# Optimization experiments

Hardware: AMD Instinct MI355X
Metric: run time of the kernel (lower is better)

The kernel has to match this reference:

```python
import jax, jax.numpy as jnp
import numpy as np

N, E, DIN, DOUT, EDIM = 100000, 1000000, 64, 64, 64


def _xavier(k, shape, gain=1.0):
    fan_out, fan_in = shape
    a = gain * np.sqrt(6.0 / (fan_in + fan_out))
    return jax.random.uniform(k, shape, jnp.float32, -a, a)


def setup_inputs() -> dict:
    key = jax.random.key(0)
    ks = jax.random.split(key, 16)
    relu_gain = float(np.sqrt(2.0))  # nn.init.calculate_gain('relu')
    return {
        "nfeats": jax.random.normal(ks[0], (N, DIN), jnp.float32),
        "efeats": jax.random.normal(ks[1], (E, EDIM), jnp.float32),
        "src": jax.random.randint(ks[2], (E,), 0, N),
        "dst": jax.random.randint(ks[3], (E,), 0, N),
        "e_perm": jax.random.permutation(ks[4], E),
        # layer 0 params (torch Linear layout: [out, in])
        "Wmsg0": _xavier(ks[5], (DOUT, DIN + EDIM)),
        "bmsg0": jnp.zeros((DOUT,), jnp.float32),
        "Wapply0": _xavier(ks[6], (DOUT, DIN + DOUT), relu_gain),
        "bapply0": jnp.zeros((DOUT,), jnp.float32),
        # layer 1 params
        "Wmsg1": _xavier(ks[7], (DOUT, DOUT + EDIM)),
        "bmsg1": jnp.zeros((DOUT,), jnp.float32),
        "Wapply1": _xavier(ks[8], (DOUT, DOUT + DOUT), relu_gain),
        "bapply1": jnp.zeros((DOUT,), jnp.float32),
    }


def _sage_layer(h, ef, src, dst, Wmsg, bmsg, Wap, bap, n_nodes):
    # message: W_msg(cat(src_h, e_h)) per edge  -> [E, dout]
    m = jnp.concatenate([h[src], ef], axis=1) @ Wmsg.T + bmsg
    # mean-reduce messages onto destination nodes
    s = jax.ops.segment_sum(m, dst, num_segments=n_nodes)
    cnt = jax.ops.segment_sum(jnp.ones((dst.shape[0],), m.dtype), dst, num_segments=n_nodes)
    h_neigh = s / jnp.maximum(cnt, 1.0)[:, None]  # zero-in-degree nodes -> 0
    return jax.nn.relu(jnp.concatenate([h, h_neigh], axis=1) @ Wap.T + bap)


def _bce_with_logits(x, target):
    # mean(log(1+exp(x)) - x*target), numerically stable via logaddexp
    return jnp.mean(jnp.logaddexp(0.0, x) - x * target)


def reference(nfeats, efeats, src, dst, e_perm,
              Wmsg0, bmsg0, Wapply0, bapply0,
              Wmsg1, bmsg1, Wapply1, bapply1):
    n_nodes = nfeats.shape[0]

    def encode(ef):
        h = _sage_layer(nfeats, ef, src, dst, Wmsg0, bmsg0, Wapply0, bapply0, n_nodes)
        h = _sage_layer(h, ef, src, dst, Wmsg1, bmsg1, Wapply1, bapply1, n_nodes)
        return h

    positive = encode(efeats)
    negative = encode(efeats[e_perm])  # corrupted view: permuted edge features
    P_LABEL, N_LABEL = 1.0, 0.0  # DGI p / n targets
    return _bce_with_logits(positive, P_LABEL) + _bce_with_logits(negative, N_LABEL)
```

## Files before the change

kernel.cpp:

```cpp
#include <hip/hip_runtime.h>
#include <math.h>

#define NN 100000
#define NE 1000000
#define D  64
#define NB_SCAN 391


__global__ __launch_bounds__(256) void k_hist(
    const int* __restrict__ dst, int* __restrict__ counts, int* __restrict__ rank)
{
    int e = blockIdx.x * 256 + threadIdx.x;
    if (e >= NE) return;
    rank[e] = atomicAdd(&counts[dst[e]], 1);
}

__global__ __launch_bounds__(256) void k_scan1(
    const int* __restrict__ counts, int* __restrict__ row_start, int* __restrict__ bsum)
{
    __shared__ int s[256];
    int t = threadIdx.x;
    int i = blockIdx.x * 256 + t;
    int v = (i < NN) ? counts[i] : 0;
    s[t] = v; __syncthreads();
#pragma unroll
    for (int off = 1; off < 256; off <<= 1) {
        int add = (t >= off) ? s[t - off] : 0;
        __syncthreads();
        s[t] += add;
        __syncthreads();
    }
    if (i < NN) row_start[i] = s[t] - v;
    if (t == 255) bsum[blockIdx.x] = s[255];
}

__global__ __launch_bounds__(512) void k_scan2(
    const int* __restrict__ bsum, int* __restrict__ boff, int* __restrict__ row_start)
{
    __shared__ int s[512];
    int t = threadIdx.x;
    int v = (t < NB_SCAN) ? bsum[t] : 0;
    s[t] = v; __syncthreads();
#pragma unroll
    for (int off = 1; off < 512; off <<= 1) {
        int add = (t >= off) ? s[t - off] : 0;
        __syncthreads();
        s[t] += add;
        __syncthreads();
    }
    if (t < NB_SCAN) boff[t] = s[t] - v;
    if (t == 0) row_start[NN] = NE;
}

__global__ __launch_bounds__(256) void k_scan3(
    int* __restrict__ row_start, const int* __restrict__ boff)
{
    int i = blockIdx.x * 256 + threadIdx.x;
    if (i < NN) row_start[i] += boff[i >> 8];
}

__global__ __launch_bounds__(256) void k_scatter(
    const int* __restrict__ dst, const int* __restrict__ src,
    const int* __restrict__ perm, const int* __restrict__ rank,
    const int* __restrict__ row_start, int4* __restrict__ sorted)
{
    int e = blockIdx.x * 256 + threadIdx.x;
    if (e >= NE) return;
    int pos = row_start[dst[e]] + rank[e];
    sorted[pos] = make_int4(src[e], e, perm[e], 0);
}


__global__ __launch_bounds__(256) void pull_pass1(
    const int4* __restrict__ sorted, const int* __restrict__ row_start,
    const float* __restrict__ nfeats, const float* __restrict__ efeats,
    float* __restrict__ hsum0, float* __restrict__ efsP, float* __restrict__ efsN)
{
    int gt = blockIdx.x * 256 + threadIdx.x;
    int w = gt >> 6, lane = gt & 63;
    if (w >= NN) return;
    int es = lane >> 4, c4 = (lane & 15) << 2;
    int beg = row_start[w], end = row_start[w + 1];

    float an0 = 0.f, an1 = 0.f, an2 = 0.f, an3 = 0.f;
    float ap0 = 0.f, ap1 = 0.f, ap2 = 0.f, ap3 = 0.f;
    float ag0 = 0.f, ag1 = 0.f, ag2 = 0.f, ag3 = 0.f;
    int i = beg + es;
    int4 q = (i < end) ? sorted[i] : make_int4(0, 0, 0, 0);
#pragma unroll 1
    for (; i < end; i += 4) {
        int inext = i + 4;
        int4 qn = (inext < end) ? sorted[inext] : make_int4(0, 0, 0, 0);
        float4 n  = *(const float4*)(nfeats + (size_t)q.x * D + c4);
        float4 ep = *(const float4*)(efeats + (size_t)q.y * D + c4);
        float4 en = *(const float4*)(efeats + (size_t)q.z * D + c4);
        an0 += n.x;  an1 += n.y;  an2 += n.z;  an3 += n.w;
        ap0 += ep.x; ap1 += ep.y; ap2 += ep.z; ap3 += ep.w;
        ag0 += en.x; ag1 += en.y; ag2 += en.z; ag3 += en.w;
        q = qn;
    }
#pragma unroll
    for (int off = 16; off <= 32; off <<= 1) {
        an0 += __shfl_xor(an0, off, 64); an1 += __shfl_xor(an1, off, 64);
        an2 += __shfl_xor(an2, off, 64); an3 += __shfl_xor(an3, off, 64);
        ap0 += __shfl_xor(ap0, off, 64); ap1 += __shfl_xor(ap1, off, 64);
        ap2 += __shfl_xor(ap2, off, 64); ap3 += __shfl_xor(ap3, off, 64);
        ag0 += __shfl_xor(ag0, off, 64); ag1 += __shfl_xor(ag1, off, 64);
        ag2 += __shfl_xor(ag2, off, 64); ag3 += __shfl_xor(ag3, off, 64);
    }
    if (lane < 16) {
        *(float4*)(hsum0 + (size_t)w * D + c4) = make_float4(an0, an1, an2, an3);
        *(float4*)(efsP  + (size_t)w * D + c4) = make_float4(ap0, ap1, ap2, ap3);
        *(float4*)(efsN  + (size_t)w * D + c4) = make_float4(ag0, ag1, ag2, ag3);
    }
}

__global__ __launch_bounds__(256) void pull_h2(
    const int4* __restrict__ sorted, const int* __restrict__ row_start,
    const float* __restrict__ hP, const float* __restrict__ hN,
    float* __restrict__ hsumP, float* __restrict__ hsumN)
{
    int gt = blockIdx.x * 256 + threadIdx.x;
    int w = gt >> 6, lane = gt & 63;
    if (w >= NN) return;
    int es = lane >> 4, c4 = (lane & 15) << 2;
    int beg = row_start[w], end = row_start[w + 1];

    float p0 = 0.f, p1 = 0.f, p2 = 0.f, p3 = 0.f;
    float n0 = 0.f, n1 = 0.f, n2 = 0.f, n3 = 0.f;
    int i = beg + es;
    int s = (i < end) ? sorted[i].x : 0;
#pragma unroll 1
    for (; i < end; i += 4) {
        int inext = i + 4;
        int sn = (inext < end) ? sorted[inext].x : 0;
        float4 vP = *(const float4*)(hP + (size_t)s * D + c4);
        float4 vN = *(const float4*)(hN + (size_t)s * D + c4);
        p0 += vP.x; p1 += vP.y; p2 += vP.z; p3 += vP.w;
        n0 += vN.x; n1 += vN.y; n2 += vN.z; n3 += vN.w;
        s = sn;
    }
#pragma unroll
    for (int off = 16; off <= 32; off <<= 1) {
        p0 += __shfl_xor(p0, off, 64); p1 += __shfl_xor(p1, off, 64);
        p2 += __shfl_xor(p2, off, 64); p3 += __shfl_xor(p3, off, 64);
        n0 += __shfl_xor(n0, off, 64); n1 += __shfl_xor(n1, off, 64);
        n2 += __shfl_xor(n2, off, 64); n3 += __shfl_xor(n3, off, 64);
    }
    if (lane < 16) {
        *(float4*)(hsumP + (size_t)w * D + c4) = make_float4(p0, p1, p2, p3);
        *(float4*)(hsumN + (size_t)w * D + c4) = make_float4(n0, n1, n2, n3);
    }
}


__device__ __forceinline__ void gemm_half(
    float acc[4][4], const float (*As)[68], const float (*Bs)[68],
    int ty, int tx4, int hb)
{
#pragma unroll 1
    for (int k0 = 0; k0 < 64; k0 += 4) {
        float a[4][4];
#pragma unroll
        for (int i = 0; i < 4; ++i)
            *(float4*)&a[i][0] = *(const float4*)&As[ty + 16 * i][k0];
#pragma unroll
        for (int kk = 0; kk < 4; ++kk) {
            float4 b = *(const float4*)&Bs[hb + k0 + kk][tx4];
#pragma unroll
            for (int i = 0; i < 4; ++i) {
                acc[i][0] += a[i][kk] * b.x;
                acc[i][1] += a[i][kk] * b.y;
                acc[i][2] += a[i][kk] * b.z;
                acc[i][3] += a[i][kk] * b.w;
            }
        }
    }
}

#define STAGE_A(SRC) { \
    _Pragma("unroll") \
    for (int g = 0; g < 4; ++g) { \
        int idx = g * 256 + tid; \
        int node = idx >> 4, c = (idx & 15) << 2; \
        int gn = block0 + node; \
        float4 v = make_float4(0.f, 0.f, 0.f, 0.f); \
        if (gn < NN) v = *(const float4*)((SRC) + (size_t)gn * D + c); \
        *(float4*)&As[node][c] = v; } }

#define STAGE_B(W) { \
    _Pragma("unroll 1") \
    for (int i = 0; i < 32; ++i) { \
        int idx = i * 256 + tid; \
        Bs[idx & 127][idx >> 7] = (W)[idx]; } }

#define STORE_MSG(M) { \
    _Pragma("unroll") \
    for (int i = 0; i < 4; ++i) \
        *(float4*)&As[ty + 16 * i][tx4] = make_float4((M)[i][0], (M)[i][1], (M)[i][2], (M)[i][3]); }

__global__ __launch_bounds__(256, 4) void fused2_l0(
    const float* __restrict__ Hsum, const float* __restrict__ EsumP,
    const float* __restrict__ EsumN, const float* __restrict__ Hprev,
    const int* __restrict__ counts,
    const float* __restrict__ Wmsg, const float* __restrict__ bmsg,
    const float* __restrict__ Wap, const float* __restrict__ bap,
    float* __restrict__ HoutP, float* __restrict__ HoutN)
{
    __shared__ __align__(16) float As[64][68];
    __shared__ __align__(16) float Bs[128][68];
    int tid = threadIdx.x;
    int block0 = blockIdx.x * 64;
    int tx = tid & 15, ty = tid >> 4;
    int tx4 = tx << 2;

    float cnt[4], inv[4];
#pragma unroll
    for (int i = 0; i < 4; ++i) {
        int gn = block0 + ty + 16 * i;
        cnt[i] = (gn < NN) ? (float)counts[gn] : 0.f;
        inv[i] = 1.0f / fmaxf(cnt[i], 1.0f);
    }
    float bm[4], ba[4];
#pragma unroll
    for (int j = 0; j < 4; ++j) { bm[j] = bmsg[tx4 + j]; ba[j] = bap[tx4 + j]; }

    STAGE_B(Wmsg);
    STAGE_A(Hsum);
    __syncthreads();
    float accb[4][4] = {};
    gemm_half(accb, As, Bs, ty, tx4, 0);
    __syncthreads();
    STAGE_A(EsumP);
    __syncthreads();
    float msgP[4][4];
#pragma unroll
    for (int i = 0; i < 4; ++i)
#pragma unroll
        for (int j = 0; j < 4; ++j) msgP[i][j] = accb[i][j];
    gemm_half(msgP, As, Bs, ty, tx4, 64);
#pragma unroll
    for (int i = 0; i < 4; ++i)
#pragma unroll
        for (int j = 0; j < 4; ++j) msgP[i][j] = (msgP[i][j] + cnt[i] * bm[j]) * inv[i];
    __syncthreads();
    STAGE_A(EsumN);
    __syncthreads();
    gemm_half(accb, As, Bs, ty, tx4, 64);
    float msgN[4][4];
#pragma unroll
    for (int i = 0; i < 4; ++i)
#pragma unroll
        for (int j = 0; j < 4; ++j) msgN[i][j] = (accb[i][j] + cnt[i] * bm[j]) * inv[i];

    __syncthreads();
    STAGE_B(Wap);
    STAGE_A(Hprev);
    __syncthreads();
    float acc2b[4][4] = {};
    gemm_half(acc2b, As, Bs, ty, tx4, 0);

    __syncthreads();
    STORE_MSG(msgP);
    __syncthreads();
    float acc2[4][4];
#pragma unroll
    for (int i = 0; i < 4; ++i)
#pragma unroll
        for (int j = 0; j < 4; ++j) acc2[i][j] = acc2b[i][j];
    gemm_half(acc2, As, Bs, ty, tx4, 64);
#pragma unroll
    for (int i = 0; i < 4; ++i) {
        int gn = block0 + ty + 16 * i;
        if (gn >= NN) continue;
#pragma unroll
        for (int j = 0; j < 4; ++j)
            HoutP[(size_t)gn * D + tx4 + j] = fmaxf(acc2[i][j] + ba[j], 0.f);
    }

    __syncthreads();
    STORE_MSG(msgN);
    __syncthreads();
#pragma unroll
    for (int i = 0; i < 4; ++i)
#pragma unroll
        for (int j = 0; j < 4; ++j) acc2[i][j] = acc2b[i][j];
    gemm_half(acc2, As, Bs, ty, tx4, 64);
#pragma unroll
    for (int i = 0; i < 4; ++i) {
        int gn = block0 + ty + 16 * i;
        if (gn >= NN) continue;
#pragma unroll
        for (int j = 0; j < 4; ++j)
            HoutN[(size_t)gn * D + tx4 + j] = fmaxf(acc2[i][j] + ba[j], 0.f);
    }
}

__global__ __launch_bounds__(256, 4) void fused2_l1loss(
    const float* __restrict__ HsumP, const float* __restrict__ HsumN,
    const float* __restrict__ EsumP, const float* __restrict__ EsumN,
    const float* __restrict__ HprevP, const float* __restrict__ HprevN,
    const int* __restrict__ counts,
    const float* __restrict__ Wmsg, const float* __restrict__ bmsg,
    const float* __restrict__ Wap, const float* __restrict__ bap,
    float* __restrict__ loss_out)
{
    __shared__ __align__(16) float As[64][68];
    __shared__ __align__(16) float Bs[128][68];
    int tid = threadIdx.x;
    int block0 = blockIdx.x * 64;
    int tx = tid & 15, ty = tid >> 4;
    int tx4 = tx << 2;

    float cnt[4], inv[4];
#pragma unroll
    for (int i = 0; i < 4; ++i) {
        int gn = block0 + ty + 16 * i;
        cnt[i] = (gn < NN) ? (float)counts[gn] : 0.f;
        inv[i] = 1.0f / fmaxf(cnt[i], 1.0f);
    }
    float bm[4], ba[4];
#pragma unroll
    for (int j = 0; j < 4; ++j) { bm[j] = bmsg[tx4 + j]; ba[j] = bap[tx4 + j]; }

    float lsum = 0.f;
#pragma unroll 1
    for (int side = 0; side < 2; ++side) {
        const float* Hsum  = side ? HsumN  : HsumP;
        const float* Esum  = side ? EsumN  : EsumP;
        const float* Hprev = side ? HprevN : HprevP;

        if (side == 0) { STAGE_B(Wmsg); }
        else {
            __syncthreads();
            STAGE_B(Wmsg);
        }
        STAGE_A(Hsum);
        __syncthreads();
        float acc[4][4] = {};
        gemm_half(acc, As, Bs, ty, tx4, 0);
        __syncthreads();
        STAGE_A(Esum);
        __syncthreads();
        gemm_half(acc, As, Bs, ty, tx4, 64);
        float msg[4][4];
#pragma unroll
        for (int i = 0; i < 4; ++i)
#pragma unroll
            for (int j = 0; j < 4; ++j) msg[i][j] = (acc[i][j] + cnt[i] * bm[j]) * inv[i];

        __syncthreads();
        STAGE_B(Wap);
        STAGE_A(Hprev);
        __syncthreads();
        float acc2[4][4] = {};
        gemm_half(acc2, As, Bs, ty, tx4, 0);
        __syncthreads();
        STORE_MSG(msg);
        __syncthreads();
        gemm_half(acc2, As, Bs, ty, tx4, 64);

#pragma unroll
        for (int i = 0; i < 4; ++i) {
            int gn = block0 + ty + 16 * i;
            if (gn >= NN) continue;
#pragma unroll
            for (int j = 0; j < 4; ++j) {
                float x = fmaxf(acc2[i][j] + ba[j], 0.f);
                float l = log1pf(expf(-x));
                if (side) l += x;
                lsum += l;
            }
        }
    }
#pragma unroll
    for (int off = 32; off; off >>= 1) lsum += __shfl_down(lsum, off, 64);
    if ((tid & 63) == 0)
        unsafeAtomicAdd(loss_out, lsum * (1.0f / 6400000.0f));
}

extern "C" void kernel_launch(void* const* d_in, const int* in_sizes, int n_in,
                              void* d_out, int out_size, void* d_ws, size_t ws_size,
                              hipStream_t stream) {
    (void)in_sizes; (void)n_in; (void)out_size; (void)ws_size;
    const float* nfeats = (const float*)d_in[0];
    const float* efeats = (const float*)d_in[1];
    const int*   src    = (const int*)d_in[2];
    const int*   dst    = (const int*)d_in[3];
    const int*   perm   = (const int*)d_in[4];
    const float* Wmsg0  = (const float*)d_in[5];
    const float* bmsg0  = (const float*)d_in[6];
    const float* Wap0   = (const float*)d_in[7];
    const float* bap0   = (const float*)d_in[8];
    const float* Wmsg1  = (const float*)d_in[9];
    const float* bmsg1  = (const float*)d_in[10];
    const float* Wap1   = (const float*)d_in[11];
    const float* bap1   = (const float*)d_in[12];
    float* out = (float*)d_out;

    const size_t NV = (size_t)NN * D;
    char* p = (char*)d_ws;
    int4* sorted   = (int4*)p;               p += (size_t)NE * 16;
    int*  rank     = (int*)p;                p += (size_t)NE * 4;
    int*  counts   = (int*)p;                p += ((NN + 15) & ~15) * 4;
    int*  rowst    = (int*)p;                p += ((NN + 16) & ~15) * 4;
    int*  bsum     = (int*)p;                p += 512 * 4;
    int*  boff     = (int*)p;                p += 512 * 4;
    float* efsP    = (float*)p;              p += NV * 4;
    float* efsN    = (float*)p;              p += NV * 4;
    float* hsum0   = (float*)p;              p += NV * 4;
    float* h1P     = (float*)p;              p += NV * 4;
    float* h1N     = (float*)p;              p += NV * 4;
    float* hsum1P  = (float*)p;              p += NV * 4;
    float* hsum1N  = (float*)p;              p += NV * 4;

    const int EGb = (NE + 255) / 256;
    const int PGb = ((size_t)NN * 64 + 255) / 256;
    const int NG  = (NN + 63) / 64;

    hipMemsetAsync(counts, 0, (size_t)NN * 4, stream);
    hipMemsetAsync(d_out, 0, 4, stream);

    k_hist<<<EGb, 256, 0, stream>>>(dst, counts, rank);
    k_scan1<<<NB_SCAN, 256, 0, stream>>>(counts, rowst, bsum);
    k_scan2<<<1, 512, 0, stream>>>(bsum, boff, rowst);
    k_scan3<<<NB_SCAN, 256, 0, stream>>>(rowst, boff);
    k_scatter<<<EGb, 256, 0, stream>>>(dst, src, perm, rank, rowst, sorted);

    pull_pass1<<<PGb, 256, 0, stream>>>(sorted, rowst, nfeats, efeats, hsum0, efsP, efsN);

    fused2_l0<<<NG, 256, 0, stream>>>(hsum0, efsP, efsN, nfeats, counts,
                                      Wmsg0, bmsg0, Wap0, bap0, h1P, h1N);

    pull_h2<<<PGb, 256, 0, stream>>>(sorted, rowst, h1P, h1N, hsum1P, hsum1N);

    fused2_l1loss<<<NG, 256, 0, stream>>>(hsum1P, hsum1N, efsP, efsN, h1P, h1N,
                                          counts, Wmsg1, bmsg1, Wap1, bap1, out);
}
```

Before: 912.9 us.

## Pre-transpose weights once and read GEMM operands directly from global memory

Adds a small kernel that transposes the four weight matrices into a k-major layout once per call. The fused node GEMM kernels drop the shared-memory B tile and most A staging, and each thread reads its A rows and B columns straight from global/L2. Only the message tile still goes through LDS. This removes the per-block 32-iteration strided weight staging, many barriers and about 35KB of LDS per block, which may raise occupancy. The cost is redundant global loads across threads, which now depend on L1/L2 hits instead of LDS reuse.

```diff
diff --git a/kernel.cpp b/kernel.cpp
--- a/kernel.cpp
+++ b/kernel.cpp
@@ -68,6 +68,20 @@
     if (e >= NE) return;
     int pos = row_start[dst[e]] + rank[e];
     sorted[pos] = make_int4(src[e], e, perm[e], 0);
+}
+
+__global__ __launch_bounds__(256) void k_wt4(
+    const float* __restrict__ W0, const float* __restrict__ W1,
+    const float* __restrict__ W2, const float* __restrict__ W3,
+    float* __restrict__ T0, float* __restrict__ T1,
+    float* __restrict__ T2, float* __restrict__ T3)
+{
+    int t = blockIdx.x * 256 + threadIdx.x;
+    int m = t >> 13, idx = t & 8191;
+    const float* W = (m == 0) ? W0 : (m == 1) ? W1 : (m == 2) ? W2 : W3;
+    float*       T = (m == 0) ? T0 : (m == 1) ? T1 : (m == 2) ? T2 : T3;
+    int j = idx >> 7, k = idx & 127;
+    T[k * 64 + j] = W[idx];
 }
 
 
@@ -154,70 +168,77 @@
 }
 
 
-__device__ __forceinline__ void gemm_half(
-    float acc[4][4], const float (*As)[68], const float (*Bs)[68],
-    int ty, int tx4, int hb)
-{
-#pragma unroll 1
+__device__ __forceinline__ void gemm_gg(
+    float acc[4][4], const float* const* Ap, const float* __restrict__ Bt)
+{
+#pragma unroll 2
     for (int k0 = 0; k0 < 64; k0 += 4) {
         float a[4][4];
+        float4 bv[4];
+#pragma unroll
+        for (int i = 0; i < 4; ++i)
+            *(float4*)&a[i][0] = *(const float4*)(Ap[i] + k0);
+#pragma unroll
+        for (int kk = 0; kk < 4; ++kk)
+            bv[kk] = *(const float4*)(Bt + (k0 + kk) * 64);
+#pragma unroll
+        for (int kk = 0; kk < 4; ++kk)
+#pragma unroll
+            for (int i = 0; i < 4; ++i) {
+                acc[i][0] += a[i][kk] * bv[kk].x;
+                acc[i][1] += a[i][kk] * bv[kk].y;
+                acc[i][2] += a[i][kk] * bv[kk].z;
+                acc[i][3] += a[i][kk] * bv[kk].w;
+            }
+    }
+}
+
+__device__ __forceinline__ void gemm_lg(
+    float acc[4][4], const float (*As)[68], int ty, const float* __restrict__ Bt)
+{
+#pragma unroll 2
+    for (int k0 = 0; k0 < 64; k0 += 4) {
+        float a[4][4];
+        float4 bv[4];
 #pragma unroll
         for (int i = 0; i < 4; ++i)
             *(float4*)&a[i][0] = *(const float4*)&As[ty + 16 * i][k0];
 #pragma unroll
-        for (int kk = 0; kk < 4; ++kk) {
-            float4 b = *(const float4*)&Bs[hb + k0 + kk][tx4];
+        for (int kk = 0; kk < 4; ++kk)
+            bv[kk] = *(const float4*)(Bt + (k0 + kk) * 64);
+#pragma unroll
+        for (int kk = 0; kk < 4; ++kk)
 #pragma unroll
             for (int i = 0; i < 4; ++i) {
-                acc[i][0] += a[i][kk] * b.x;
-                acc[i][1] += a[i][kk] * b.y;
-                acc[i][2] += a[i][kk] * b.z;
-                acc[i][3] += a[i][kk] * b.w;
+                acc[i][0] += a[i][kk] * bv[kk].x;
+                acc[i][1] += a[i][kk] * bv[kk].y;
+                acc[i][2] += a[i][kk] * bv[kk].z;
+                acc[i][3] += a[i][kk] * bv[kk].w;
             }
-        }
-    }
-}
-
-#define STAGE_A(SRC) { \
-    _Pragma("unroll") \
-    for (int g = 0; g < 4; ++g) { \
-        int idx = g * 256 + tid; \
-        int node = idx >> 4, c = (idx & 15) << 2; \
-        int gn = block0 + node; \
-        float4 v = make_float4(0.f, 0.f, 0.f, 0.f); \
-        if (gn < NN) v = *(const float4*)((SRC) + (size_t)gn * D + c); \
-        *(float4*)&As[node][c] = v; } }
-
-#define STAGE_B(W) { \
-    _Pragma("unroll 1") \
-    for (int i = 0; i < 32; ++i) { \
-        int idx = i * 256 + tid; \
-        Bs[idx & 127][idx >> 7] = (W)[idx]; } }
-
-#define STORE_MSG(M) { \
-    _Pragma("unroll") \
-    for (int i = 0; i < 4; ++i) \
-        *(float4*)&As[ty + 16 * i][tx4] = make_float4((M)[i][0], (M)[i][1], (M)[i][2], (M)[i][3]); }
-
-__global__ __launch_bounds__(256, 4) void fused2_l0(
+    }
+}
+
+__global__ __launch_bounds__(256, 4) void fused3_l0(
     const float* __restrict__ Hsum, const float* __restrict__ EsumP,
     const float* __restrict__ EsumN, const float* __restrict__ Hprev,
     const int* __restrict__ counts,
-    const float* __restrict__ Wmsg, const float* __restrict__ bmsg,
-    const float* __restrict__ Wap, const float* __restrict__ bap,
+    const float* __restrict__ WtM, const float* __restrict__ bmsg,
+    const float* __restrict__ WtA, const float* __restrict__ bap,
     float* __restrict__ HoutP, float* __restrict__ HoutN)
 {
     __shared__ __align__(16) float As[64][68];
-    __shared__ __align__(16) float Bs[128][68];
     int tid = threadIdx.x;
     int block0 = blockIdx.x * 64;
     int tx = tid & 15, ty = tid >> 4;
     int tx4 = tx << 2;
 
+    size_t off[4];
     float cnt[4], inv[4];
 #pragma unroll
     for (int i = 0; i < 4; ++i) {
         int gn = block0 + ty + 16 * i;
+        int rc = (gn < NN) ? gn : (NN - 1);
+        off[i] = (size_t)rc * D;
         cnt[i] = (gn < NN) ? (float)counts[gn] : 0.f;
         inv[i] = 1.0f / fmaxf(cnt[i], 1.0f);
     }
@@ -225,50 +246,43 @@
 #pragma unroll
     for (int j = 0; j < 4; ++j) { bm[j] = bmsg[tx4 + j]; ba[j] = bap[tx4 + j]; }
 
-    STAGE_B(Wmsg);
-    STAGE_A(Hsum);
-    __syncthreads();
+    const float* BtM = WtM + tx4;
+    const float* BtA = WtA + tx4;
+    const float* Ap[4];
+
     float accb[4][4] = {};
-    gemm_half(accb, As, Bs, ty, tx4, 0);
-    __syncthreads();
-    STAGE_A(EsumP);
-    __syncthreads();
+#pragma unroll
+    for (int i = 0; i < 4; ++i) Ap[i] = Hsum + off[i];
+    gemm_gg(accb, Ap, BtM);
+
     float msgP[4][4];
 #pragma unroll
     for (int i = 0; i < 4; ++i)
 #pragma unroll
         for (int j = 0; j < 4; ++j) msgP[i][j] = accb[i][j];
-    gemm_half(msgP, As, Bs, ty, tx4, 64);
+#pragma unroll
+    for (int i = 0; i < 4; ++i) Ap[i] = EsumP + off[i];
+    gemm_gg(msgP, Ap, BtM + 64 * 64);
 #pragma unroll
     for (int i = 0; i < 4; ++i)
 #pragma unroll
         for (int j = 0; j < 4; ++j) msgP[i][j] = (msgP[i][j] + cnt[i] * bm[j]) * inv[i];
-    __syncthreads();
-    STAGE_A(EsumN);
-    __syncthreads();
-    gemm_half(accb, As, Bs, ty, tx4, 64);
-    float msgN[4][4];
-#pragma unroll
-    for (int i = 0; i < 4; ++i)
-#pragma unroll
-        for (int j = 0; j < 4; ++j) msgN[i][j] = (accb[i][j] + cnt[i] * bm[j]) * inv[i];
-
-    __syncthreads();
-    STAGE_B(Wap);
-    STAGE_A(Hprev);
-    __syncthreads();
+#pragma unroll
+    for (int i = 0; i < 4; ++i)
+        *(float4*)&As[ty + 16 * i][tx4] = make_float4(msgP[i][0], msgP[i][1], msgP[i][2], msgP[i][3]);
+
     float acc2b[4][4] = {};
-    gemm_half(acc2b, As, Bs, ty, tx4, 0);
-
-    __syncthreads();
-    STORE_MSG(msgP);
+#pragma unroll
+    for (int i = 0; i < 4; ++i) Ap[i] = Hprev + off[i];
+    gemm_gg(acc2b, Ap, BtA);
+
     __syncthreads();
     float acc2[4][4];
 #pragma unroll
     for (int i = 0; i < 4; ++i)
 #pragma unroll
         for (int j = 0; j < 4; ++j) acc2[i][j] = acc2b[i][j];
-    gemm_half(acc2, As, Bs, ty, tx4, 64);
+    gemm_lg(acc2, As, ty, BtA + 64 * 64);
 #pragma unroll
     for (int i = 0; i < 4; ++i) {
         int gn = block0 + ty + 16 * i;
@@ -278,14 +292,24 @@
             HoutP[(size_t)gn * D + tx4 + j] = fmaxf(acc2[i][j] + ba[j], 0.f);
     }
 
+#pragma unroll
+    for (int i = 0; i < 4; ++i) Ap[i] = EsumN + off[i];
+    gemm_gg(accb, Ap, BtM + 64 * 64);
+#pragma unroll
+    for (int i = 0; i < 4; ++i)
+#pragma unroll
+        for (int j = 0; j < 4; ++j) accb[i][j] = (accb[i][j] + cnt[i] * bm[j]) * inv[i];
+
     __syncthreads();
-    STORE_MSG(msgN);
+#pragma unroll
+    for (int i = 0; i < 4; ++i)
+        *(float4*)&As[ty + 16 * i][tx4] = make_float4(accb[i][0], accb[i][1], accb[i][2], accb[i][3]);
     __syncthreads();
 #pragma unroll
     for (int i = 0; i < 4; ++i)
 #pragma unroll
         for (int j = 0; j < 4; ++j) acc2[i][j] = acc2b[i][j];
-    gemm_half(acc2, As, Bs, ty, tx4, 64);
+    gemm_lg(acc2, As, ty, BtA + 64 * 64);
 #pragma unroll
     for (int i = 0; i < 4; ++i) {
         int gn = block0 + ty + 16 * i;
@@ -296,32 +320,38 @@
     }
 }
 
-__global__ __launch_bounds__(256, 4) void fused2_l1loss(
+__global__ __launch_bounds__(256, 4) void fused3_l1loss(
     const float* __restrict__ HsumP, const float* __restrict__ HsumN,
     const float* __restrict__ EsumP, const float* __restrict__ EsumN,
     const float* __restrict__ HprevP, const float* __restrict__ HprevN,
     const int* __restrict__ counts,
-    const float* __restrict__ Wmsg, const float* __restrict__ bmsg,
-    const float* __restrict__ Wap, const float* __restrict__ bap,
+    const float* __restrict__ WtM, const float* __restrict__ bmsg,
+    const float* __restrict__ WtA, const float* __restrict__ bap,
     float* __restrict__ loss_out)
 {
     __shared__ __align__(16) float As[64][68];
-    __shared__ __align__(16) float Bs[128][68];
     int tid = threadIdx.x;
     int block0 = blockIdx.x * 64;
     int tx = tid & 15, ty = tid >> 4;
     int tx4 = tx << 2;
 
+    size_t off[4];
     float cnt[4], inv[4];
 #pragma unroll
     for (int i = 0; i < 4; ++i) {
         int gn = block0 + ty + 16 * i;
+        int rc = (gn < NN) ? gn : (NN - 1);
+        off[i] = (size_t)rc * D;
         cnt[i] = (gn < NN) ? (float)counts[gn] : 0.f;
         inv[i] = 1.0f / fmaxf(cnt[i], 1.0f);
     }
     float bm[4], ba[4];
 #pragma unroll
     for (int j = 0; j < 4; ++j) { bm[j] = bmsg[tx4 + j]; ba[j] = bap[tx4 + j]; }
+
+    const float* BtM = WtM + tx4;
+    const float* BtA = WtA + tx4;
+    const float* Ap[4];
 
     float lsum = 0.f;
 #pragma unroll 1
@@ -330,35 +360,30 @@
         const float* Esum  = side ? EsumN  : EsumP;
         const float* Hprev = side ? HprevN : HprevP;
 
-        if (side == 0) { STAGE_B(Wmsg); }
-        else {
-            __syncthreads();
-            STAGE_B(Wmsg);
-        }
-        STAGE_A(Hsum);
-        __syncthreads();
         float acc[4][4] = {};
-        gemm_half(acc, As, Bs, ty, tx4, 0);
-        __syncthreads();
-        STAGE_A(Esum);
-        __syncthreads();
-        gemm_half(acc, As, Bs, ty, tx4, 64);
+#pragma unroll
+        for (int i = 0; i < 4; ++i) Ap[i] = Hsum + off[i];
+        gemm_gg(acc, Ap, BtM);
+#pragma unroll
+        for (int i = 0; i < 4; ++i) Ap[i] = Esum + off[i];
+        gemm_gg(acc, Ap, BtM + 64 * 64);
         float msg[4][4];
 #pragma unroll
         for (int i = 0; i < 4; ++i)
 #pragma unroll
             for (int j = 0; j < 4; ++j) msg[i][j] = (acc[i][j] + cnt[i] * bm[j]) * inv[i];
 
-        __syncthreads();
-        STAGE_B(Wap);
-        STAGE_A(Hprev);
-        __syncthreads();
         float acc2[4][4] = {};
-        gemm_half(acc2, As, Bs, ty, tx4, 0);
-        __syncthreads();
-        STORE_MSG(msg);
-        __syncthreads();
-        gemm_half(acc2, As, Bs, ty, tx4, 64);
+#pragma unroll
+        for (int i = 0; i < 4; ++i) Ap[i] = Hprev + off[i];
+        gemm_gg(acc2, Ap, BtA);
+
+        __syncthreads();
+#pragma unroll
+        for (int i = 0; i < 4; ++i)
+            *(float4*)&As[ty + 16 * i][tx4] = make_float4(msg[i][0], msg[i][1], msg[i][2], msg[i][3]);
+        __syncthreads();
+        gemm_lg(acc2, As, ty, BtA + 64 * 64);
 
 #pragma unroll
         for (int i = 0; i < 4; ++i) {
@@ -374,7 +399,7 @@
         }
     }
 #pragma unroll
-    for (int off = 32; off; off >>= 1) lsum += __shfl_down(lsum, off, 64);
+    for (int off2 = 32; off2; off2 >>= 1) lsum += __shfl_down(lsum, off2, 64);
     if ((tid & 63) == 0)
         unsafeAtomicAdd(loss_out, lsum * (1.0f / 6400000.0f));
 }
@@ -413,6 +438,10 @@
     float* h1N     = (float*)p;              p += NV * 4;
     float* hsum1P  = (float*)p;              p += NV * 4;
     float* hsum1N  = (float*)p;              p += NV * 4;
+    float* wtM0    = (float*)p;              p += 8192 * 4;
+    float* wtA0    = (float*)p;              p += 8192 * 4;
+    float* wtM1    = (float*)p;              p += 8192 * 4;
+    float* wtA1    = (float*)p;              p += 8192 * 4;
 
     const int EGb = (NE + 255) / 256;
     const int PGb = ((size_t)NN * 64 + 255) / 256;
@@ -420,6 +449,8 @@
 
     hipMemsetAsync(counts, 0, (size_t)NN * 4, stream);
     hipMemsetAsync(d_out, 0, 4, stream);
+
+    k_wt4<<<128, 256, 0, stream>>>(Wmsg0, Wap0, Wmsg1, Wap1, wtM0, wtA0, wtM1, wtA1);
 
     k_hist<<<EGb, 256, 0, stream>>>(dst, counts, rank);
     k_scan1<<<NB_SCAN, 256, 0, stream>>>(counts, rowst, bsum);
@@ -429,11 +460,11 @@
 
     pull_pass1<<<PGb, 256, 0, stream>>>(sorted, rowst, nfeats, efeats, hsum0, efsP, efsN);
 
-    fused2_l0<<<NG, 256, 0, stream>>>(hsum0, efsP, efsN, nfeats, counts,
-                                      Wmsg0, bmsg0, Wap0, bap0, h1P, h1N);
+    fused3_l0<<<NG, 256, 0, stream>>>(hsum0, efsP, efsN, nfeats, counts,
+                                      wtM0, bmsg0, wtA0, bap0, h1P, h1N);
 
     pull_h2<<<PGb, 256, 0, stream>>>(sorted, rowst, h1P, h1N, hsum1P, hsum1N);
 
-    fused2_l1loss<<<NG, 256, 0, stream>>>(hsum1P, hsum1N, efsP, efsN, h1P, h1N,
-                                          counts, Wmsg1, bmsg1, Wap1, bap1, out);
-}
+    fused3_l1loss<<<NG, 256, 0, stream>>>(hsum1P, hsum1N, efsP, efsN, h1P, h1N,
+                                          counts, wtM1, bmsg1, wtA1, bap1, out);
+}
```

Result: slower. 1.015 ms (+11.1%).

## Pre-transpose weights once and stage half-sized B tiles to cut LDS

Applied to the files above, without the earlier changes.

Adds a small kernel that transposes all four weight matrices into a [k][j] layout in workspace once per call. The fused GEMM kernels then load each 64-row half of the weights with coalesced float4 copies into a B tile half the previous size, instead of doing strided scalar transposing stores of the full 128x64 matrix. This lowers LDS per block, which may raise occupancy, and makes weight staging cheaper. The cost is extra syncs and restaging between halves, and one more kernel launch. The inner GEMM loop also preloads four B vectors ahead of the FMAs.

```diff
diff --git a/kernel.cpp b/kernel.cpp
--- a/kernel.cpp
+++ b/kernel.cpp
@@ -68,6 +68,20 @@
     if (e >= NE) return;
     int pos = row_start[dst[e]] + rank[e];
     sorted[pos] = make_int4(src[e], e, perm[e], 0);
+}
+
+__global__ __launch_bounds__(256) void k_wt4(
+    const float* __restrict__ W0, const float* __restrict__ W1,
+    const float* __restrict__ W2, const float* __restrict__ W3,
+    float* __restrict__ T0, float* __restrict__ T1,
+    float* __restrict__ T2, float* __restrict__ T3)
+{
+    int t = blockIdx.x * 256 + threadIdx.x;
+    int m = t >> 13, idx = t & 8191;
+    const float* W = (m == 0) ? W0 : (m == 1) ? W1 : (m == 2) ? W2 : W3;
+    float*       T = (m == 0) ? T0 : (m == 1) ? T1 : (m == 2) ? T2 : T3;
+    int j = idx >> 7, k = idx & 127;
+    T[k * 64 + j] = W[idx];
 }
 
 
@@ -154,27 +168,29 @@
 }
 
 
-__device__ __forceinline__ void gemm_half(
+__device__ __forceinline__ void gemm_h(
     float acc[4][4], const float (*As)[68], const float (*Bs)[68],
-    int ty, int tx4, int hb)
+    int ty, int tx4)
 {
 #pragma unroll 1
     for (int k0 = 0; k0 < 64; k0 += 4) {
         float a[4][4];
+        float4 bv[4];
 #pragma unroll
         for (int i = 0; i < 4; ++i)
             *(float4*)&a[i][0] = *(const float4*)&As[ty + 16 * i][k0];
 #pragma unroll
-        for (int kk = 0; kk < 4; ++kk) {
-            float4 b = *(const float4*)&Bs[hb + k0 + kk][tx4];
+        for (int kk = 0; kk < 4; ++kk)
+            bv[kk] = *(const float4*)&Bs[k0 + kk][tx4];
+#pragma unroll
+        for (int kk = 0; kk < 4; ++kk)
 #pragma unroll
             for (int i = 0; i < 4; ++i) {
-                acc[i][0] += a[i][kk] * b.x;
-                acc[i][1] += a[i][kk] * b.y;
-                acc[i][2] += a[i][kk] * b.z;
-                acc[i][3] += a[i][kk] * b.w;
+                acc[i][0] += a[i][kk] * bv[kk].x;
+                acc[i][1] += a[i][kk] * bv[kk].y;
+                acc[i][2] += a[i][kk] * bv[kk].z;
+                acc[i][3] += a[i][kk] * bv[kk].w;
             }
-        }
     }
 }
 
@@ -188,27 +204,28 @@
         if (gn < NN) v = *(const float4*)((SRC) + (size_t)gn * D + c); \
         *(float4*)&As[node][c] = v; } }
 
-#define STAGE_B(W) { \
-    _Pragma("unroll 1") \
-    for (int i = 0; i < 32; ++i) { \
-        int idx = i * 256 + tid; \
-        Bs[idx & 127][idx >> 7] = (W)[idx]; } }
+#define STAGE_BH(WT, HALF) { \
+    _Pragma("unroll") \
+    for (int g = 0; g < 4; ++g) { \
+        int m = g * 256 + tid; \
+        *(float4*)&Bs[m >> 4][(m & 15) << 2] = \
+            *(const float4*)((WT) + (HALF) * 4096 + m * 4); } }
 
 #define STORE_MSG(M) { \
     _Pragma("unroll") \
     for (int i = 0; i < 4; ++i) \
         *(float4*)&As[ty + 16 * i][tx4] = make_float4((M)[i][0], (M)[i][1], (M)[i][2], (M)[i][3]); }
 
-__global__ __launch_bounds__(256, 4) void fused2_l0(
+__global__ __launch_bounds__(256, 4) void fused4_l0(
     const float* __restrict__ Hsum, const float* __restrict__ EsumP,
     const float* __restrict__ EsumN, const float* __restrict__ Hprev,
     const int* __restrict__ counts,
-    const float* __restrict__ Wmsg, const float* __restrict__ bmsg,
-    const float* __restrict__ Wap, const float* __restrict__ bap,
+    const float* __restrict__ WtM, const float* __restrict__ bmsg,
+    const float* __restrict__ WtA, const float* __restrict__ bap,
     float* __restrict__ HoutP, float* __restrict__ HoutN)
 {
     __shared__ __align__(16) float As[64][68];
-    __shared__ __align__(16) float Bs[128][68];
+    __shared__ __align__(16) float Bs[64][68];
     int tid = threadIdx.x;
     int block0 = blockIdx.x * 64;
     int tx = tid & 15, ty = tid >> 4;
@@ -225,12 +242,14 @@
 #pragma unroll
     for (int j = 0; j < 4; ++j) { bm[j] = bmsg[tx4 + j]; ba[j] = bap[tx4 + j]; }
 
-    STAGE_B(Wmsg);
+    STAGE_BH(WtM, 0);
     STAGE_A(Hsum);
     __syncthreads();
     float accb[4][4] = {};
-    gemm_half(accb, As, Bs, ty, tx4, 0);
-    __syncthreads();
+    gemm_h(accb, As, Bs, ty, tx4);
+
+    __syncthreads();
+    STAGE_BH(WtM, 1);
     STAGE_A(EsumP);
     __syncthreads();
     float msgP[4][4];
@@ -238,29 +257,30 @@
     for (int i = 0; i < 4; ++i)
 #pragma unroll
         for (int j = 0; j < 4; ++j) msgP[i][j] = accb[i][j];
-    gemm_half(msgP, As, Bs, ty, tx4, 64);
+    gemm_h(msgP, As, Bs, ty, tx4);
 #pragma unroll
     for (int i = 0; i < 4; ++i)
 #pragma unroll
         for (int j = 0; j < 4; ++j) msgP[i][j] = (msgP[i][j] + cnt[i] * bm[j]) * inv[i];
+
     __syncthreads();
     STAGE_A(EsumN);
     __syncthreads();
-    gemm_half(accb, As, Bs, ty, tx4, 64);
-    float msgN[4][4];
+    gemm_h(accb, As, Bs, ty, tx4);
 #pragma unroll
     for (int i = 0; i < 4; ++i)
 #pragma unroll
-        for (int j = 0; j < 4; ++j) msgN[i][j] = (accb[i][j] + cnt[i] * bm[j]) * inv[i];
-
-    __syncthreads();
-    STAGE_B(Wap);
+        for (int j = 0; j < 4; ++j) accb[i][j] = (accb[i][j] + cnt[i] * bm[j]) * inv[i];
+
+    __syncthreads();
+    STAGE_BH(WtA, 0);
     STAGE_A(Hprev);
     __syncthreads();
     float acc2b[4][4] = {};
-    gemm_half(acc2b, As, Bs, ty, tx4, 0);
-
-    __syncthreads();
+    gemm_h(acc2b, As, Bs, ty, tx4);
+
+    __syncthreads();
+    STAGE_BH(WtA, 1);
     STORE_MSG(msgP);
     __syncthreads();
     float acc2[4][4];
@@ -268,7 +288,7 @@
     for (int i = 0; i < 4; ++i)
 #pragma unroll
         for (int j = 0; j < 4; ++j) acc2[i][j] = acc2b[i][j];
-    gemm_half(acc2, As, Bs, ty, tx4, 64);
+    gemm_h(acc2, As, Bs, ty, tx4);
 #pragma unroll
     for (int i = 0; i < 4; ++i) {
         int gn = block0 + ty + 16 * i;
@@ -279,13 +299,13 @@
     }
 
     __syncthreads();
-    STORE_MSG(msgN);
+    STORE_MSG(accb);
     __syncthreads();
 #pragma unroll
     for (int i = 0; i < 4; ++i)
 #pragma unroll
         for (int j = 0; j < 4; ++j) acc2[i][j] = acc2b[i][j];
-    gemm_half(acc2, As, Bs, ty, tx4, 64);
+    gemm_h(acc2, As, Bs, ty, tx4);
 #pragma unroll
     for (int i = 0; i < 4; ++i) {
         int gn = block0 + ty + 16 * i;
@@ -296,17 +316,17 @@
     }
 }
 
-__global__ __launch_bounds__(256, 4) void fused2_l1loss(
+__global__ __launch_bounds__(256, 4) void fused4_l1loss(
     const float* __restrict__ HsumP, const float* __restrict__ HsumN,
     const float* __restrict__ EsumP, const float* __restrict__ EsumN,
     const float* __restrict__ HprevP, const float* __restrict__ HprevN,
     const int* __restrict__ counts,
-    const float* __restrict__ Wmsg, const float* __restrict__ bmsg,
-    const float* __restrict__ Wap, const float* __restrict__ bap,
+    const float* __restrict__ WtM, const float* __restrict__ bmsg,
+    const float* __restrict__ WtA, const float* __restrict__ bap,
     float* __restrict__ loss_out)
 {
     __shared__ __align__(16) float As[64][68];
-    __shared__ __align__(16) float Bs[128][68];
+    __shared__ __align__(16) float Bs[64][68];
     int tid = threadIdx.x;
     int block0 = blockIdx.x * 64;
     int tx = tid & 15, ty = tid >> 4;
@@ -330,19 +350,18 @@
         const float* Esum  = side ? EsumN  : EsumP;
         const float* Hprev = side ? HprevN : HprevP;
 
-        if (side == 0) { STAGE_B(Wmsg); }
-        else {
-            __syncthreads();
-            STAGE_B(Wmsg);
-        }
+        __syncthreads();
+        STAGE_BH(WtM, 0);
         STAGE_A(Hsum);
         __syncthreads();
         float acc[4][4] = {};
-        gemm_half(acc, As, Bs, ty, tx4, 0);
-        __syncthreads();
+        gemm_h(acc, As, Bs, ty, tx4);
+
+        __syncthreads();
+        STAGE_BH(WtM, 1);
         STAGE_A(Esum);
         __syncthreads();
-        gemm_half(acc, As, Bs, ty, tx4, 64);
+        gemm_h(acc, As, Bs, ty, tx4);
         float msg[4][4];
 #pragma unroll
         for (int i = 0; i < 4; ++i)
@@ -350,15 +369,17 @@
             for (int j = 0; j < 4; ++j) msg[i][j] = (acc[i][j] + cnt[i] * bm[j]) * inv[i];
 
         __syncthreads();
-        STAGE_B(Wap);
+        STAGE_BH(WtA, 0);
         STAGE_A(Hprev);
         __syncthreads();
         float acc2[4][4] = {};
-        gemm_half(acc2, As, Bs, ty, tx4, 0);
-        __syncthreads();
+        gemm_h(acc2, As, Bs, ty, tx4);
+
+        __syncthreads();
+        STAGE_BH(WtA, 1);
         STORE_MSG(msg);
         __syncthreads();
-        gemm_half(acc2, As, Bs, ty, tx4, 64);
+        gemm_h(acc2, As, Bs, ty, tx4);
 
 #pragma unroll
         for (int i = 0; i < 4; ++i) {
@@ -374,7 +395,7 @@
         }
     }
 #pragma unroll
-    for (int off = 32; off; off >>= 1) lsum += __shfl_down(lsum, off, 64);
+    for (int off2 = 32; off2; off2 >>= 1) lsum += __shfl_down(lsum, off2, 64);
     if ((tid & 63) == 0)
         unsafeAtomicAdd(loss_out, lsum * (1.0f / 6400000.0f));
 }
@@ -413,6 +434,10 @@
     float* h1N     = (float*)p;              p += NV * 4;
     float* hsum1P  = (float*)p;              p += NV * 4;
     float* hsum1N  = (float*)p;              p += NV * 4;
+    float* wtM0    = (float*)p;              p += 8192 * 4;
+    float* wtA0    = (float*)p;              p += 8192 * 4;
+    float* wtM1    = (float*)p;              p += 8192 * 4;
+    float* wtA1    = (float*)p;              p += 8192 * 4;
 
     const int EGb = (NE + 255) / 256;
     const int PGb = ((size_t)NN * 64 + 255) / 256;
@@ -420,6 +445,8 @@
 
     hipMemsetAsync(counts, 0, (size_t)NN * 4, stream);
     hipMemsetAsync(d_out, 0, 4, stream);
+
+    k_wt4<<<128, 256, 0, stream>>>(Wmsg0, Wap0, Wmsg1, Wap1, wtM0, wtA0, wtM1, wtA1);
 
     k_hist<<<EGb, 256, 0, stream>>>(dst, counts, rank);
     k_scan1<<<NB_SCAN, 256, 0, stream>>>(counts, rowst, bsum);
@@ -429,11 +456,11 @@
 
     pull_pass1<<<PGb, 256, 0, stream>>>(sorted, rowst, nfeats, efeats, hsum0, efsP, efsN);
 
-    fused2_l0<<<NG, 256, 0, stream>>>(hsum0, efsP, efsN, nfeats, counts,
-                                      Wmsg0, bmsg0, Wap0, bap0, h1P, h1N);
+    fused4_l0<<<NG, 256, 0, stream>>>(hsum0, efsP, efsN, nfeats, counts,
+                                      wtM0, bmsg0, wtA0, bap0, h1P, h1N);
 
     pull_h2<<<PGb, 256, 0, stream>>>(sorted, rowst, h1P, h1N, hsum1P, hsum1N);
 
-    fused2_l1loss<<<NG, 256, 0, stream>>>(hsum1P, hsum1N, efsP, efsN, h1P, h1N,
-                                          counts, Wmsg1, bmsg1, Wap1, bap1, out);
-}
+    fused4_l1loss<<<NG, 256, 0, stream>>>(hsum1P, hsum1N, efsP, efsN, h1P, h1N,
+                                          counts, wtM1, bmsg1, wtA1, bap1, out);
+}
```

Result: faster. 870.2 us (-4.7%).
